# Optimization experiments

Hardware: AMD Instinct MI355X
Metric: run time of the kernel (lower is better)

The kernel has to match this reference:

```python
import jax, jax.numpy as jnp
import numpy as np

SR = 44100
D = SR * 30          # duration_samples = 1_323_000
N = 1024             # number of note events
L = 32768            # max note length in samples
W = 1024             # hann window length (module's window_length)
H = 8                # harmonics in the synth
K = 128              # FIR taps in the effect chain
LAT = 2              # time_latent_size


def setup_inputs() -> dict:
    key = jax.random.key(0)
    ks = jax.random.split(key, 10)
    freq_rad = jax.random.uniform(ks[0], (N,), jnp.float32, 0.01, 0.3)
    velocity = jax.random.uniform(ks[1], (N,), jnp.float32, 1.0, 127.0)
    starts = jax.random.randint(ks[2], (N,), 0, D - L, dtype=jnp.int32)
    lengths = jax.random.randint(ks[3], (N,), 2048, L + 1, dtype=jnp.int32)
    # time_embedder: Linear(1,32) -> ReLU -> Linear(32,LAT)
    w1 = jax.random.normal(ks[4], (1, 32), jnp.float32)
    b1 = jnp.zeros((32,), jnp.float32)
    w2 = jax.random.normal(ks[5], (32, LAT), jnp.float32) / jnp.sqrt(32.0)
    b2 = jnp.zeros((LAT,), jnp.float32)
    # synth amplitude MLP: [freq, vel, latent] (2+LAT) -> 64 -> H
    ws1 = jax.random.normal(ks[6], (2 + LAT, 64), jnp.float32)
    bs1 = jnp.zeros((64,), jnp.float32)
    ws2 = jax.random.normal(ks[7], (64, H), jnp.float32) / 8.0
    bs2 = jnp.zeros((H,), jnp.float32)
    # effect chain: causal FIR (OIW layout) + tanh
    fir = jax.random.normal(ks[8], (1, 1, K), jnp.float32) / K
    return dict(freq_rad=freq_rad, velocity=velocity,
                w1=w1, b1=b1, w2=w2, b2=b2,
                ws1=ws1, bs1=bs1, ws2=ws2, bs2=bs2, fir=fir,
                starts=starts, lengths=lengths, duration_samples=D)


def reference(freq_rad, velocity, w1, b1, w2, b2, ws1, bs1, ws2, bs2, fir,
              starts, lengths, duration_samples):
    Dn = int(duration_samples)
    t = jnp.arange(L, dtype=jnp.float32)            # [L]
    ti = jnp.arange(L, dtype=jnp.int32)             # [L]
    ends = starts + lengths
    # output_length = min(end, duration) - start, clipped to [0, L]
    out_len = jnp.clip(jnp.minimum(ends, Dn) - starts, 0, L)  # [N]
    # time latent: MLP on normalized start time
    nt = (starts.astype(jnp.float32) / Dn)[:, None]           # [N,1]
    lat = jax.nn.relu(nt @ w1 + b1) @ w2 + b2                  # [N,LAT]
    vel = (velocity / 127.0)[:, None]                          # [N,1]
    # harmonic amplitudes from tiny MLP (the 'synth')
    feat = jnp.concatenate([freq_rad[:, None], vel, lat], axis=-1)  # [N,2+LAT]
    amps = jax.nn.softplus(jax.nn.relu(feat @ ws1 + bs1) @ ws2 + bs2)  # [N,H]
    # additive synthesis; fixed small loop over harmonics, vectorized over [N,L]
    phase = freq_rad[:, None] * t[None, :]                     # [N,L]
    seg = jnp.zeros((N, L), jnp.float32)
    for hh in range(1, H + 1):
        seg = seg + amps[:, hh - 1:hh] * jnp.sin(hh * phase)
    seg = seg * vel
    # hann window (torch periodic) on the LAST W samples of each variable-length segment
    n = jnp.arange(W, dtype=jnp.float32)
    hann = 0.5 * (1.0 - jnp.cos(2.0 * jnp.pi * n / W))         # [W]
    wpos = ti[None, :] - (out_len[:, None] - W)                # [N,L]
    in_win = (wpos >= 0) & (wpos < W)
    factor = jnp.where(in_win, hann[jnp.clip(wpos, 0, W - 1)], 1.0)
    mask = (ti[None, :] < out_len[:, None]).astype(jnp.float32)  # zero past segment end
    seg = seg * factor * mask
    # effect chain: causal 128-tap FIR then tanh (masked so padding stays silent)
    y = jax.lax.conv_general_dilated(seg[:, None, :], fir,
                                     window_strides=(1,), padding=[(K - 1, 0)])
    seg = jnp.tanh(y[:, 0, :]) * mask                          # [N,L]
    # overlap-add: scatter each note into the output buffer
    idx = starts[:, None] + ti[None, :]                        # [N,L]
    valid = (ti[None, :] < out_len[:, None]) & (idx < Dn)
    contrib = jnp.where(valid, seg, 0.0)
    out = jnp.zeros((Dn,), jnp.float32).at[jnp.clip(idx, 0, Dn - 1).reshape(-1)].add(
        contrib.reshape(-1))
    return out
```

## Files before the change

kernel.cpp:

```cpp
#include <hip/hip_runtime.h>
#include <math.h>

#define LMAX  32768
#define WWIN  1024
#define KFIR  128
#define WOUT  1024
#define TO    1024
#define CPAD  1232
#define SYNTH 1152
#define ZPS   1148
#define SLOT  128

typedef _Float16 v8h __attribute__((ext_vector_type(8)));
typedef _Float16 v4h __attribute__((ext_vector_type(4)));
typedef float    v4f __attribute__((ext_vector_type(4)));
typedef float    v2f __attribute__((ext_vector_type(2)));

__device__ __forceinline__ float fast_tanh(float x) {
    float e = __builtin_amdgcn_exp2f(x * 2.8853900817779268f);
    return fmaf(-2.0f, __builtin_amdgcn_rcpf(e + 1.0f), 1.0f);
}

__global__ __launch_bounds__(256) void setup_notes_k(
    const float* __restrict__ freq_g, const float* __restrict__ velo_g,
    const float* __restrict__ w1,  const float* __restrict__ b1,
    const float* __restrict__ w2,  const float* __restrict__ b2,
    const float* __restrict__ ws1, const float* __restrict__ bs1,
    const float* __restrict__ ws2, const float* __restrict__ bs2,
    const int* __restrict__ starts, const int* __restrict__ lengths,
    float* __restrict__ npar, int* __restrict__ counts,
    unsigned short* __restrict__ lists,
    int Dn, int N, int n_tiles)
{
    __shared__ float s_w1[32], s_b1[32], s_w2[64], s_b2[2];
    __shared__ float s_ws1[256], s_bs1[64], s_ws2[512], s_bs2[8];
    const int tid = threadIdx.x;
    if (tid < 32) { s_w1[tid] = w1[tid]; s_b1[tid] = b1[tid]; }
    if (tid < 64) { s_w2[tid] = w2[tid]; s_bs1[tid] = bs1[tid]; }
    if (tid < 2)  s_b2[tid] = b2[tid];
    if (tid < 8)  s_bs2[tid] = bs2[tid];
    s_ws1[tid] = ws1[tid];
    s_ws2[tid] = ws2[tid];  s_ws2[tid + 256] = ws2[tid + 256];
    __syncthreads();

    const int j = blockIdx.x * 256 + tid;
    if (j >= N) return;

    int st  = starts[j];
    int len = lengths[j];
    int ol  = min(st + len, Dn) - st;
    ol = max(0, min(ol, LMAX));
    float v = velo_g[j] * (1.0f / 127.0f);
    float f = freq_g[j];
    float nt = (float)st / (float)Dn;
    float lat0 = s_b2[0], lat1 = s_b2[1];
    #pragma unroll
    for (int jj = 0; jj < 32; ++jj) {
        float h = fmaxf(fmaf(nt, s_w1[jj], s_b1[jj]), 0.0f);
        lat0 = fmaf(h, s_w2[jj * 2 + 0], lat0);
        lat1 = fmaf(h, s_w2[jj * 2 + 1], lat1);
    }
    float acc[8];
    #pragma unroll
    for (int h = 0; h < 8; ++h) acc[h] = s_bs2[h];
    #pragma unroll
    for (int jj = 0; jj < 64; ++jj) {
        float a = s_bs1[jj];
        a = fmaf(f,    s_ws1[0 * 64 + jj], a);
        a = fmaf(v,    s_ws1[1 * 64 + jj], a);
        a = fmaf(lat0, s_ws1[2 * 64 + jj], a);
        a = fmaf(lat1, s_ws1[3 * 64 + jj], a);
        a = fmaxf(a, 0.0f);
        #pragma unroll
        for (int h = 0; h < 8; ++h)
            acc[h] = fmaf(a, s_ws2[jj * 8 + h], acc[h]);
    }
    float* p = npar + (size_t)j * 12;
    p[0] = __int_as_float(st);
    p[1] = __int_as_float(ol);
    p[2] = f;
    p[3] = 0.0f;
    #pragma unroll
    for (int h = 0; h < 8; ++h) {
        float a = acc[h];
        float sp = fmaxf(a, 0.0f) + log1pf(expf(-fabsf(a)));
        p[4 + h] = sp * v;
    }

    if (ol > 0) {
        int t0 = st >> 10;
        int t1 = min((st + ol - 1) >> 10, n_tiles - 1);
        for (int t = t0; t <= t1; ++t) {
            int pos = atomicAdd(&counts[t], 1);
            if (pos < SLOT) lists[(size_t)t * SLOT + pos] = (unsigned short)j;
        }
    }
}

__global__ __launch_bounds__(1024) void sort_tiles_k(
    const int* __restrict__ counts, int* __restrict__ order, int n_tiles)
{
    __shared__ int hist[SLOT + 2];
    __shared__ int bstart[SLOT + 2];
    const int tid = threadIdx.x;
    if (tid < SLOT + 2) hist[tid] = 0;
    __syncthreads();
    for (int t = tid; t < n_tiles; t += 1024) {
        int k = min(counts[t], SLOT + 1);
        atomicAdd(&hist[k], 1);
    }
    __syncthreads();
    if (tid == 0) {
        int run = 0;
        for (int k = SLOT + 1; k >= 0; --k) { bstart[k] = run; run += hist[k]; }
    }
    __syncthreads();
    for (int t = tid; t < n_tiles; t += 1024) {
        int k = min(counts[t], SLOT + 1);
        int p = atomicAdd(&bstart[k], 1);
        order[p] = t;
    }
}

__global__ __launch_bounds__(256, 3) void synth_fused_k(
    const float* __restrict__ fir,
    const float* __restrict__ npar,
    const int* __restrict__ counts,
    const unsigned short* __restrict__ lists,
    const int* __restrict__ order,
    float* __restrict__ out, int Dn)
{
    __shared__ __align__(16) _Float16 segc[4][4][CPAD];
    __shared__ float fir_s[KFIR];
    __shared__ int   stl[SLOT], oll[SLOT];
    __shared__ float fl[SLOT];
    __shared__ __align__(16) float ampsl[SLOT][8];

    const int tid  = threadIdx.x;
    const int wid  = tid >> 6;
    const int lane = tid & 63;
    const int m    = lane & 15;
    const int quad = lane >> 4;
    const int grp  = wid;
    const int tile = order[blockIdx.x];
    const int o0   = tile * TO;
    const int ow   = o0;

    const int K = min(counts[tile], SLOT);

    if (tid < KFIR) fir_s[tid] = fir[tid];
    if (tid < K) {
        const int nid = (int)lists[(size_t)tile * SLOT + tid];
        const float4* pp = (const float4*)(npar + (size_t)nid * 12);
        float4 a = pp[0], b = pp[1], c = pp[2];
        stl[tid] = __float_as_int(a.x);
        oll[tid] = __float_as_int(a.y);
        fl[tid]  = a.z;
        *(float4*)&ampsl[tid][0] = b;
        *(float4*)&ampsl[tid][4] = c;
    }
    __syncthreads();

    v8h afrag[12];
    #pragma unroll
    for (int t = 0; t < 12; ++t) {
        v8h af;
        #pragma unroll
        for (int j = 0; j < 8; ++j) {
            int idx = 32 * t + 8 * quad + j - 16 * m;
            float fv = (idx >= 0 && idx < KFIR) ? fir_s[idx] : 0.0f;
            af[j] = (_Float16)fv;
        }
        afrag[t] = af;
    }
    for (int z = lane; z < 4 * (CPAD - ZPS); z += 64) {
        int S = z / (CPAD - ZPS), off = z % (CPAD - ZPS);
        segc[wid][S][ZPS + off] = (_Float16)0.0f;
    }

    const _Float16* __restrict__ bbase = &segc[wid][m & 3][(m & ~3) + 8 * quad];

    float accv[16];
    #pragma unroll
    for (int r = 0; r < 16; ++r) accv[r] = 0.0f;

    const double inv2pi = 0.15915494309189535;

    int stN = 0, olN = 0; float fN = 0.f;
    float4 amN0 = {}, amN1 = {};
    if (grp < K) {
        stN = stl[grp]; olN = oll[grp]; fN = fl[grp];
        amN0 = *(const float4*)&ampsl[grp][0];
        amN1 = *(const float4*)&ampsl[grp][4];
    }

    for (int kk = grp; kk < K; kk += 4) {
        const int st = stN, ol = olN;
        const float f = fN;
        const float4 am0 = amN0, am1 = amN1;
        if (kk + 4 < K) {
            stN = stl[kk + 4]; olN = oll[kk + 4]; fN = fl[kk + 4];
            amN0 = *(const float4*)&ampsl[kk + 4][0];
            amN1 = *(const float4*)&ampsl[kk + 4][4];
        }

        const int base = ow - st;
        if (base >= ol || base + WOUT <= 0) continue;

        const v2f A0v = {am0.x, am0.x}, A1v = {am0.y, am0.y};
        const v2f A2v = {am0.z, am0.z}, A3v = {am0.w, am0.w};
        const v2f A4v = {am1.x, am1.x}, A5v = {am1.y, am1.y};
        const v2f A6v = {am1.z, am1.z}, A7v = {am1.w, am1.w};
        const double fd = (double)f;

        const int tseed = base - 127 + lane;
        double rev0 = fd * (double)tseed * inv2pi;
        double d64  = fd * 64.0 * inv2pi;
        double rev1 = rev0 + d64;
        double d128 = d64 + d64;
        float r0   = (float)(rev0 - floor(rev0));
        float r1   = (float)(rev1 - floor(rev1));
        float r128 = (float)(d128 - floor(d128));
        v2f s  = { __builtin_amdgcn_sinf(r0), __builtin_amdgcn_sinf(r1) };
        v2f cc = { __builtin_amdgcn_cosf(r0), __builtin_amdgcn_cosf(r1) };
        const float sd128 = __builtin_amdgcn_sinf(r128);
        const float cd128 = __builtin_amdgcn_cosf(r128);
        const v2f sdv = {sd128, sd128}, cdv = {cd128, cd128};
        const int wbase = ol - WWIN;

        const bool interior = (base >= 127) && (base + WOUT + 1 <= wbase);

        if (interior) {
            #pragma unroll
            for (int j = 0; j < SYNTH / 128; ++j) {
                v2f tc = cc + cc;
                v2f sA = s;
                v2f sum = sA * A0v;
                v2f sB = tc * sA;                                 sum = __builtin_elementwise_fma(A1v, sB, sum);
                v2f sC = __builtin_elementwise_fma(tc, sB, -sA);  sum = __builtin_elementwise_fma(A2v, sC, sum);
                v2f sD = __builtin_elementwise_fma(tc, sC, -sB);  sum = __builtin_elementwise_fma(A3v, sD, sum);
                v2f sE = __builtin_elementwise_fma(tc, sD, -sC);  sum = __builtin_elementwise_fma(A4v, sE, sum);
                v2f sF = __builtin_elementwise_fma(tc, sE, -sD);  sum = __builtin_elementwise_fma(A5v, sF, sum);
                v2f sG = __builtin_elementwise_fma(tc, sF, -sE);  sum = __builtin_elementwise_fma(A6v, sG, sum);
                v2f sH = __builtin_elementwise_fma(tc, sG, -sF);  sum = __builtin_elementwise_fma(A7v, sH, sum);
                _Float16 h0 = (_Float16)sum.x;
                _Float16 h1 = (_Float16)sum.y;
                const int x0 = lane + 128 * j;
                const int x1 = x0 + 64;
                if (j == 0) {
                    #pragma unroll
                    for (int S = 0; S < 4; ++S)
                        if (x0 >= S) segc[wid][S][x0 - S] = h0;
                } else {
                    #pragma unroll
                    for (int S = 0; S < 4; ++S)
                        segc[wid][S][x0 - S] = h0;
                }
                #pragma unroll
                for (int S = 0; S < 4; ++S)
                    segc[wid][S][x1 - S] = h1;
                v2f ns = __builtin_elementwise_fma(s, cdv, cc * sdv);
                v2f nc = __builtin_elementwise_fma(cc, cdv, -(s * sdv));
                s = ns; cc = nc;
            }
        } else {
            #pragma unroll
            for (int j = 0; j < SYNTH / 128; ++j) {
                const int t0 = tseed + 128 * j;
                const int t1 = t0 + 64;
                v2f tc = cc + cc;
                v2f sA = s;
                v2f sum = sA * A0v;
                v2f sB = tc * sA;                                 sum = __builtin_elementwise_fma(A1v, sB, sum);
                v2f sC = __builtin_elementwise_fma(tc, sB, -sA);  sum = __builtin_elementwise_fma(A2v, sC, sum);
                v2f sD = __builtin_elementwise_fma(tc, sC, -sB);  sum = __builtin_elementwise_fma(A3v, sD, sum);
                v2f sE = __builtin_elementwise_fma(tc, sD, -sC);  sum = __builtin_elementwise_fma(A4v, sE, sum);
                v2f sF = __builtin_elementwise_fma(tc, sE, -sD);  sum = __builtin_elementwise_fma(A5v, sF, sum);
                v2f sG = __builtin_elementwise_fma(tc, sF, -sE);  sum = __builtin_elementwise_fma(A6v, sG, sum);
                v2f sH = __builtin_elementwise_fma(tc, sG, -sF);  sum = __builtin_elementwise_fma(A7v, sH, sum);
                float v0 = 0.0f, v1 = 0.0f;
                if (t0 >= 0 && t0 < ol) {
                    float factor = 1.0f;
                    int wpos = t0 - wbase;
                    if (wpos >= 0)
                        factor = 0.5f - 0.5f * __builtin_amdgcn_cosf((float)wpos * (1.0f / WWIN));
                    v0 = sum.x * factor;
                }
                if (t1 >= 0 && t1 < ol) {
                    float factor = 1.0f;
                    int wpos = t1 - wbase;
                    if (wpos >= 0)
                        factor = 0.5f - 0.5f * __builtin_amdgcn_cosf((float)wpos * (1.0f / WWIN));
                    v1 = sum.y * factor;
                }
                _Float16 h0 = (_Float16)v0;
                _Float16 h1 = (_Float16)v1;
                const int x0 = lane + 128 * j;
                const int x1 = x0 + 64;
                if (j == 0) {
                    #pragma unroll
                    for (int S = 0; S < 4; ++S)
                        if (x0 >= S) segc[wid][S][x0 - S] = h0;
                } else {
                    #pragma unroll
                    for (int S = 0; S < 4; ++S)
                        segc[wid][S][x0 - S] = h0;
                }
                #pragma unroll
                for (int S = 0; S < 4; ++S)
                    segc[wid][S][x1 - S] = h1;
                v2f ns = __builtin_elementwise_fma(s, cdv, cc * sdv);
                v2f nc = __builtin_elementwise_fma(cc, cdv, -(s * sdv));
                s = ns; cc = nc;
            }
        }

        #pragma unroll
        for (int p = 0; p < 2; ++p) {
            const int co = 512 * p;
            v4f CA0 = {0.f, 0.f, 0.f, 0.f};
            v4f CA1 = {0.f, 0.f, 0.f, 0.f};
            v4f CB0 = {0.f, 0.f, 0.f, 0.f};
            v4f CB1 = {0.f, 0.f, 0.f, 0.f};
            #pragma unroll
            for (int t = 0; t < 6; ++t) {
                v4h lo = *(const v4h*)(bbase + co + 32 * t);
                v4h hi = *(const v4h*)(bbase + co + 32 * t + 4);
                v8h bf = __builtin_shufflevector(lo, hi, 0, 1, 2, 3, 4, 5, 6, 7);
                CA0 = __builtin_amdgcn_mfma_f32_16x16x32_f16(afrag[t], bf, CA0, 0, 0, 0);
                v4h lo2 = *(const v4h*)(bbase + co + 256 + 32 * t);
                v4h hi2 = *(const v4h*)(bbase + co + 256 + 32 * t + 4);
                v8h bf2 = __builtin_shufflevector(lo2, hi2, 0, 1, 2, 3, 4, 5, 6, 7);
                CB0 = __builtin_amdgcn_mfma_f32_16x16x32_f16(afrag[t], bf2, CB0, 0, 0, 0);
            }
            #pragma unroll
            for (int t = 6; t < 12; ++t) {
                v4h lo = *(const v4h*)(bbase + co + 32 * t);
                v4h hi = *(const v4h*)(bbase + co + 32 * t + 4);
                v8h bf = __builtin_shufflevector(lo, hi, 0, 1, 2, 3, 4, 5, 6, 7);
                CA1 = __builtin_amdgcn_mfma_f32_16x16x32_f16(afrag[t], bf, CA1, 0, 0, 0);
                v4h lo2 = *(const v4h*)(bbase + co + 256 + 32 * t);
                v4h hi2 = *(const v4h*)(bbase + co + 256 + 32 * t + 4);
                v8h bf2 = __builtin_shufflevector(lo2, hi2, 0, 1, 2, 3, 4, 5, 6, 7);
                CB1 = __builtin_amdgcn_mfma_f32_16x16x32_f16(afrag[t], bf2, CB1, 0, 0, 0);
            }

            const int tb = base + co + 64 * quad + m;
            float y;
            y = CA0[0] + CA1[0]; if (tb +   0 >= 0 && tb +   0 < ol) accv[p*8+0] += fast_tanh(y);
            y = CA0[1] + CA1[1]; if (tb +  16 >= 0 && tb +  16 < ol) accv[p*8+1] += fast_tanh(y);
            y = CA0[2] + CA1[2]; if (tb +  32 >= 0 && tb +  32 < ol) accv[p*8+2] += fast_tanh(y);
            y = CA0[3] + CA1[3]; if (tb +  48 >= 0 && tb +  48 < ol) accv[p*8+3] += fast_tanh(y);
            y = CB0[0] + CB1[0]; if (tb + 256 >= 0 && tb + 256 < ol) accv[p*8+4] += fast_tanh(y);
            y = CB0[1] + CB1[1]; if (tb + 272 >= 0 && tb + 272 < ol) accv[p*8+5] += fast_tanh(y);
            y = CB0[2] + CB1[2]; if (tb + 288 >= 0 && tb + 288 < ol) accv[p*8+6] += fast_tanh(y);
            y = CB0[3] + CB1[3]; if (tb + 304 >= 0 && tb + 304 < ol) accv[p*8+7] += fast_tanh(y);
        }
    }

    __syncthreads();
    float* red = (float*)&segc[0][0][0];
    const int slot0 = 64 * quad + m;
    if (grp != 0) {
        float* rg = red + (grp - 1) * 1024;
        #pragma unroll
        for (int p = 0; p < 2; ++p) {
            #pragma unroll
            for (int r = 0; r < 8; ++r) {
                const int idx = slot0 + 512 * p + (r >> 2) * 256 + (r & 3) * 16;
                rg[idx] = accv[p * 8 + r];
            }
        }
    }
    __syncthreads();
    if (grp == 0) {
        #pragma unroll
        for (int p = 0; p < 2; ++p) {
            #pragma unroll
            for (int r = 0; r < 8; ++r) {
                const int idx = slot0 + 512 * p + (r >> 2) * 256 + (r & 3) * 16;
                float v = accv[p * 8 + r] + red[idx] + red[1024 + idx] + red[2048 + idx];
                const int ob = o0 + idx;
                if (ob < Dn) out[ob] = v;
            }
        }
    }
}

extern "C" void kernel_launch(void* const* d_in, const int* in_sizes, int n_in,
                              void* d_out, int out_size, void* d_ws, size_t ws_size,
                              hipStream_t stream) {
    const float* freq    = (const float*)d_in[0];
    const float* velo    = (const float*)d_in[1];
    const float* w1      = (const float*)d_in[2];
    const float* b1      = (const float*)d_in[3];
    const float* w2      = (const float*)d_in[4];
    const float* b2      = (const float*)d_in[5];
    const float* ws1     = (const float*)d_in[6];
    const float* bs1     = (const float*)d_in[7];
    const float* ws2     = (const float*)d_in[8];
    const float* bs2     = (const float*)d_in[9];
    const float* fir     = (const float*)d_in[10];
    const int*   starts  = (const int*)d_in[11];
    const int*   lengths = (const int*)d_in[12];

    const int N  = in_sizes[0];
    const int Dn = out_size;
    float* out = (float*)d_out;

    const int n_tiles = (Dn + TO - 1) / TO;

    char* ws = (char*)d_ws;
    float* npar = (float*)ws;
    size_t off1 = ((size_t)N * 12 * sizeof(float) + 255) & ~(size_t)255;
    int* counts = (int*)(ws + off1);
    size_t off2 = off1 + (((size_t)n_tiles * sizeof(int) + 255) & ~(size_t)255);
    unsigned short* lists = (unsigned short*)(ws + off2);
    size_t off3 = off2 + (((size_t)n_tiles * SLOT * sizeof(unsigned short) + 255) & ~(size_t)255);
    int* order = (int*)(ws + off3);

    hipMemsetAsync(counts, 0, (size_t)n_tiles * sizeof(int), stream);
    setup_notes_k<<<(N + 255) / 256, 256, 0, stream>>>(
        freq, velo, w1, b1, w2, b2, ws1, bs1, ws2, bs2,
        starts, lengths, npar, counts, lists, Dn, N, n_tiles);
    sort_tiles_k<<<1, 1024, 0, stream>>>(counts, order, n_tiles);
    synth_fused_k<<<n_tiles, 256, 0, stream>>>(
        fir, npar, counts, lists, order, out, Dn);
}
```

Measured before the change: 150.1 us.

## Split each note's synthesis and FIR across all four waves with double-buffered LDS

Before, each wave processed its own subset of notes over the full 1024-sample tile and the waves were combined by a shared-memory reduction at the end. Now all four waves work on every note together: each synthesizes an interleaved share of the 128-sample chunks and convolves its own 256-output quarter. A double-buffered segment buffer with one block barrier per note keeps writers and readers apart. This removes the final cross-wave reduction, roughly halves LDS use and allows a launch bound of 4 blocks, in exchange for a __syncthreads on every note and less independent work per wave between barriers.

```diff
diff --git a/kernel.cpp b/kernel.cpp
--- a/kernel.cpp
+++ b/kernel.cpp
@@ -4,7 +4,6 @@
 #define LMAX  32768
 #define WWIN  1024
 #define KFIR  128
-#define WOUT  1024
 #define TO    1024
 #define CPAD  1232
 #define SYNTH 1152
@@ -122,7 +121,7 @@
     }
 }
 
-__global__ __launch_bounds__(256, 3) void synth_fused_k(
+__global__ __launch_bounds__(256, 4) void synth_fused_k(
     const float* __restrict__ fir,
     const float* __restrict__ npar,
     const int* __restrict__ counts,
@@ -130,7 +129,7 @@
     const int* __restrict__ order,
     float* __restrict__ out, int Dn)
 {
-    __shared__ __align__(16) _Float16 segc[4][4][CPAD];
+    __shared__ __align__(16) _Float16 segc[2][4][CPAD];
     __shared__ float fir_s[KFIR];
     __shared__ int   stl[SLOT], oll[SLOT];
     __shared__ float fl[SLOT];
@@ -141,10 +140,9 @@
     const int lane = tid & 63;
     const int m    = lane & 15;
     const int quad = lane >> 4;
-    const int grp  = wid;
     const int tile = order[blockIdx.x];
     const int o0   = tile * TO;
-    const int ow   = o0;
+    const int co   = 256 * wid;
 
     const int K = min(counts[tile], SLOT);
 
@@ -173,218 +171,192 @@
         }
         afrag[t] = af;
     }
-    for (int z = lane; z < 4 * (CPAD - ZPS); z += 64) {
-        int S = z / (CPAD - ZPS), off = z % (CPAD - ZPS);
-        segc[wid][S][ZPS + off] = (_Float16)0.0f;
-    }
-
-    const _Float16* __restrict__ bbase = &segc[wid][m & 3][(m & ~3) + 8 * quad];
-
-    float accv[16];
-    #pragma unroll
-    for (int r = 0; r < 16; ++r) accv[r] = 0.0f;
-
+    for (int z = tid; z < 2 * 4 * (CPAD - ZPS); z += 256) {
+        int b = z / (4 * (CPAD - ZPS));
+        int r = z % (4 * (CPAD - ZPS));
+        int S = r / (CPAD - ZPS), off = r % (CPAD - ZPS);
+        segc[b][S][ZPS + off] = (_Float16)0.0f;
+    }
+
+    const _Float16* __restrict__ bb0 = &segc[0][m & 3][(m & ~3) + 8 * quad];
+    const _Float16* __restrict__ bb1 = &segc[1][m & 3][(m & ~3) + 8 * quad];
+
+    float accv[4] = {0.f, 0.f, 0.f, 0.f};
     const double inv2pi = 0.15915494309189535;
+    int cur = 0;
 
     int stN = 0, olN = 0; float fN = 0.f;
     float4 amN0 = {}, amN1 = {};
-    if (grp < K) {
-        stN = stl[grp]; olN = oll[grp]; fN = fl[grp];
-        amN0 = *(const float4*)&ampsl[grp][0];
-        amN1 = *(const float4*)&ampsl[grp][4];
-    }
-
-    for (int kk = grp; kk < K; kk += 4) {
+    if (K > 0) {
+        stN = stl[0]; olN = oll[0]; fN = fl[0];
+        amN0 = *(const float4*)&ampsl[0][0];
+        amN1 = *(const float4*)&ampsl[0][4];
+    }
+
+    const int nj = (wid == 0) ? 3 : 2;
+
+    for (int kk = 0; kk < K; ++kk) {
         const int st = stN, ol = olN;
         const float f = fN;
         const float4 am0 = amN0, am1 = amN1;
-        if (kk + 4 < K) {
-            stN = stl[kk + 4]; olN = oll[kk + 4]; fN = fl[kk + 4];
-            amN0 = *(const float4*)&ampsl[kk + 4][0];
-            amN1 = *(const float4*)&ampsl[kk + 4][4];
-        }
-
-        const int base = ow - st;
-        if (base >= ol || base + WOUT <= 0) continue;
+        if (kk + 1 < K) {
+            stN = stl[kk + 1]; olN = oll[kk + 1]; fN = fl[kk + 1];
+            amN0 = *(const float4*)&ampsl[kk + 1][0];
+            amN1 = *(const float4*)&ampsl[kk + 1][4];
+        }
+
+        const int base = o0 - st;
+        if (base >= ol || base + TO <= 0) continue;
 
         const v2f A0v = {am0.x, am0.x}, A1v = {am0.y, am0.y};
         const v2f A2v = {am0.z, am0.z}, A3v = {am0.w, am0.w};
         const v2f A4v = {am1.x, am1.x}, A5v = {am1.y, am1.y};
         const v2f A6v = {am1.z, am1.z}, A7v = {am1.w, am1.w};
         const double fd = (double)f;
-
-        const int tseed = base - 127 + lane;
-        double rev0 = fd * (double)tseed * inv2pi;
+        const int wbase = ol - WWIN;
+
+        const int tseed0 = base - 127 + lane + 128 * wid;
+        double rev0 = fd * (double)tseed0 * inv2pi;
         double d64  = fd * 64.0 * inv2pi;
         double rev1 = rev0 + d64;
-        double d128 = d64 + d64;
+        double d512 = fd * 512.0 * inv2pi;
         float r0   = (float)(rev0 - floor(rev0));
         float r1   = (float)(rev1 - floor(rev1));
-        float r128 = (float)(d128 - floor(d128));
+        float r512 = (float)(d512 - floor(d512));
         v2f s  = { __builtin_amdgcn_sinf(r0), __builtin_amdgcn_sinf(r1) };
         v2f cc = { __builtin_amdgcn_cosf(r0), __builtin_amdgcn_cosf(r1) };
-        const float sd128 = __builtin_amdgcn_sinf(r128);
-        const float cd128 = __builtin_amdgcn_cosf(r128);
-        const v2f sdv = {sd128, sd128}, cdv = {cd128, cd128};
-        const int wbase = ol - WWIN;
-
-        const bool interior = (base >= 127) && (base + WOUT + 1 <= wbase);
+        const float sd = __builtin_amdgcn_sinf(r512);
+        const float cd = __builtin_amdgcn_cosf(r512);
+        const v2f sdv = {sd, sd}, cdv = {cd, cd};
+
+        const bool interior = (base >= 127) && (base + TO + 1 <= wbase);
 
         if (interior) {
             #pragma unroll
-            for (int j = 0; j < SYNTH / 128; ++j) {
-                v2f tc = cc + cc;
-                v2f sA = s;
-                v2f sum = sA * A0v;
-                v2f sB = tc * sA;                                 sum = __builtin_elementwise_fma(A1v, sB, sum);
-                v2f sC = __builtin_elementwise_fma(tc, sB, -sA);  sum = __builtin_elementwise_fma(A2v, sC, sum);
-                v2f sD = __builtin_elementwise_fma(tc, sC, -sB);  sum = __builtin_elementwise_fma(A3v, sD, sum);
-                v2f sE = __builtin_elementwise_fma(tc, sD, -sC);  sum = __builtin_elementwise_fma(A4v, sE, sum);
-                v2f sF = __builtin_elementwise_fma(tc, sE, -sD);  sum = __builtin_elementwise_fma(A5v, sF, sum);
-                v2f sG = __builtin_elementwise_fma(tc, sF, -sE);  sum = __builtin_elementwise_fma(A6v, sG, sum);
-                v2f sH = __builtin_elementwise_fma(tc, sG, -sF);  sum = __builtin_elementwise_fma(A7v, sH, sum);
-                _Float16 h0 = (_Float16)sum.x;
-                _Float16 h1 = (_Float16)sum.y;
-                const int x0 = lane + 128 * j;
-                const int x1 = x0 + 64;
-                if (j == 0) {
+            for (int i = 0; i < 3; ++i) {
+                if (i < nj) {
+                    const int j = wid + 4 * i;
+                    v2f tc = cc + cc;
+                    v2f sA = s;
+                    v2f sum = sA * A0v;
+                    v2f sB = tc * sA;                                 sum = __builtin_elementwise_fma(A1v, sB, sum);
+                    v2f sC = __builtin_elementwise_fma(tc, sB, -sA);  sum = __builtin_elementwise_fma(A2v, sC, sum);
+                    v2f sD = __builtin_elementwise_fma(tc, sC, -sB);  sum = __builtin_elementwise_fma(A3v, sD, sum);
+                    v2f sE = __builtin_elementwise_fma(tc, sD, -sC);  sum = __builtin_elementwise_fma(A4v, sE, sum);
+                    v2f sF = __builtin_elementwise_fma(tc, sE, -sD);  sum = __builtin_elementwise_fma(A5v, sF, sum);
+                    v2f sG = __builtin_elementwise_fma(tc, sF, -sE);  sum = __builtin_elementwise_fma(A6v, sG, sum);
+                    v2f sH = __builtin_elementwise_fma(tc, sG, -sF);  sum = __builtin_elementwise_fma(A7v, sH, sum);
+                    _Float16 h0 = (_Float16)sum.x;
+                    _Float16 h1 = (_Float16)sum.y;
+                    const int x0 = lane + 128 * j;
+                    const int x1 = x0 + 64;
+                    if (i == 0) {
+                        #pragma unroll
+                        for (int S = 0; S < 4; ++S)
+                            if (x0 >= S) segc[cur][S][x0 - S] = h0;
+                    } else {
+                        #pragma unroll
+                        for (int S = 0; S < 4; ++S)
+                            segc[cur][S][x0 - S] = h0;
+                    }
                     #pragma unroll
                     for (int S = 0; S < 4; ++S)
-                        if (x0 >= S) segc[wid][S][x0 - S] = h0;
-                } else {
-                    #pragma unroll
-                    for (int S = 0; S < 4; ++S)
-                        segc[wid][S][x0 - S] = h0;
+                        segc[cur][S][x1 - S] = h1;
+                    v2f ns = __builtin_elementwise_fma(s, cdv, cc * sdv);
+                    v2f nc = __builtin_elementwise_fma(cc, cdv, -(s * sdv));
+                    s = ns; cc = nc;
                 }
-                #pragma unroll
-                for (int S = 0; S < 4; ++S)
-                    segc[wid][S][x1 - S] = h1;
-                v2f ns = __builtin_elementwise_fma(s, cdv, cc * sdv);
-                v2f nc = __builtin_elementwise_fma(cc, cdv, -(s * sdv));
-                s = ns; cc = nc;
             }
         } else {
             #pragma unroll
-            for (int j = 0; j < SYNTH / 128; ++j) {
-                const int t0 = tseed + 128 * j;
-                const int t1 = t0 + 64;
-                v2f tc = cc + cc;
-                v2f sA = s;
-                v2f sum = sA * A0v;
-                v2f sB = tc * sA;                                 sum = __builtin_elementwise_fma(A1v, sB, sum);
-                v2f sC = __builtin_elementwise_fma(tc, sB, -sA);  sum = __builtin_elementwise_fma(A2v, sC, sum);
-                v2f sD = __builtin_elementwise_fma(tc, sC, -sB);  sum = __builtin_elementwise_fma(A3v, sD, sum);
-                v2f sE = __builtin_elementwise_fma(tc, sD, -sC);  sum = __builtin_elementwise_fma(A4v, sE, sum);
-                v2f sF = __builtin_elementwise_fma(tc, sE, -sD);  sum = __builtin_elementwise_fma(A5v, sF, sum);
-                v2f sG = __builtin_elementwise_fma(tc, sF, -sE);  sum = __builtin_elementwise_fma(A6v, sG, sum);
-                v2f sH = __builtin_elementwise_fma(tc, sG, -sF);  sum = __builtin_elementwise_fma(A7v, sH, sum);
-                float v0 = 0.0f, v1 = 0.0f;
-                if (t0 >= 0 && t0 < ol) {
-                    float factor = 1.0f;
-                    int wpos = t0 - wbase;
-                    if (wpos >= 0)
-                        factor = 0.5f - 0.5f * __builtin_amdgcn_cosf((float)wpos * (1.0f / WWIN));
-                    v0 = sum.x * factor;
-                }
-                if (t1 >= 0 && t1 < ol) {
-                    float factor = 1.0f;
-                    int wpos = t1 - wbase;
-                    if (wpos >= 0)
-                        factor = 0.5f - 0.5f * __builtin_amdgcn_cosf((float)wpos * (1.0f / WWIN));
-                    v1 = sum.y * factor;
-                }
-                _Float16 h0 = (_Float16)v0;
-                _Float16 h1 = (_Float16)v1;
-                const int x0 = lane + 128 * j;
-                const int x1 = x0 + 64;
-                if (j == 0) {
+            for (int i = 0; i < 3; ++i) {
+                if (i < nj) {
+                    const int j = wid + 4 * i;
+                    const int t0 = tseed0 + 512 * i;
+                    const int t1 = t0 + 64;
+                    v2f tc = cc + cc;
+                    v2f sA = s;
+                    v2f sum = sA * A0v;
+                    v2f sB = tc * sA;                                 sum = __builtin_elementwise_fma(A1v, sB, sum);
+                    v2f sC = __builtin_elementwise_fma(tc, sB, -sA);  sum = __builtin_elementwise_fma(A2v, sC, sum);
+                    v2f sD = __builtin_elementwise_fma(tc, sC, -sB);  sum = __builtin_elementwise_fma(A3v, sD, sum);
+                    v2f sE = __builtin_elementwise_fma(tc, sD, -sC);  sum = __builtin_elementwise_fma(A4v, sE, sum);
+                    v2f sF = __builtin_elementwise_fma(tc, sE, -sD);  sum = __builtin_elementwise_fma(A5v, sF, sum);
+                    v2f sG = __builtin_elementwise_fma(tc, sF, -sE);  sum = __builtin_elementwise_fma(A6v, sG, sum);
+                    v2f sH = __builtin_elementwise_fma(tc, sG, -sF);  sum = __builtin_elementwise_fma(A7v, sH, sum);
+                    float v0 = 0.0f, v1 = 0.0f;
+                    if (t0 >= 0 && t0 < ol) {
+                        float factor = 1.0f;
+                        int wpos = t0 - wbase;
+                        if (wpos >= 0)
+                            factor = 0.5f - 0.5f * __builtin_amdgcn_cosf((float)wpos * (1.0f / WWIN));
+                        v0 = sum.x * factor;
+                    }
+                    if (t1 >= 0 && t1 < ol) {
+                        float factor = 1.0f;
+                        int wpos = t1 - wbase;
+                        if (wpos >= 0)
+                            factor = 0.5f - 0.5f * __builtin_amdgcn_cosf((float)wpos * (1.0f / WWIN));
+                        v1 = sum.y * factor;
+                    }
+                    _Float16 h0 = (_Float16)v0;
+                    _Float16 h1 = (_Float16)v1;
+                    const int x0 = lane + 128 * j;
+                    const int x1 = x0 + 64;
+                    if (i == 0) {
+                        #pragma unroll
+                        for (int S = 0; S < 4; ++S)
+                            if (x0 >= S) segc[cur][S][x0 - S] = h0;
+                    } else {
+                        #pragma unroll
+                        for (int S = 0; S < 4; ++S)
+                            segc[cur][S][x0 - S] = h0;
+                    }
                     #pragma unroll
                     for (int S = 0; S < 4; ++S)
-                        if (x0 >= S) segc[wid][S][x0 - S] = h0;
-                } else {
-                    #pragma unroll
-                    for (int S = 0; S < 4; ++S)
-                        segc[wid][S][x0 - S] = h0;
+                        segc[cur][S][x1 - S] = h1;
+                    v2f ns = __builtin_elementwise_fma(s, cdv, cc * sdv);
+                    v2f nc = __builtin_elementwise_fma(cc, cdv, -(s * sdv));
+                    s = ns; cc = nc;
                 }
-                #pragma unroll
-                for (int S = 0; S < 4; ++S)
-                    segc[wid][S][x1 - S] = h1;
-                v2f ns = __builtin_elementwise_fma(s, cdv, cc * sdv);
-                v2f nc = __builtin_elementwise_fma(cc, cdv, -(s * sdv));
-                s = ns; cc = nc;
             }
         }
 
+        __syncthreads();
+
+        const _Float16* __restrict__ bb = cur ? bb1 : bb0;
+        v4f CA0 = {0.f, 0.f, 0.f, 0.f};
+        v4f CA1 = {0.f, 0.f, 0.f, 0.f};
         #pragma unroll
-        for (int p = 0; p < 2; ++p) {
-            const int co = 512 * p;
-            v4f CA0 = {0.f, 0.f, 0.f, 0.f};
-            v4f CA1 = {0.f, 0.f, 0.f, 0.f};
-            v4f CB0 = {0.f, 0.f, 0.f, 0.f};
-            v4f CB1 = {0.f, 0.f, 0.f, 0.f};
-            #pragma unroll
-            for (int t = 0; t < 6; ++t) {
-                v4h lo = *(const v4h*)(bbase + co + 32 * t);
-                v4h hi = *(const v4h*)(bbase + co + 32 * t + 4);
-                v8h bf = __builtin_shufflevector(lo, hi, 0, 1, 2, 3, 4, 5, 6, 7);
-                CA0 = __builtin_amdgcn_mfma_f32_16x16x32_f16(afrag[t], bf, CA0, 0, 0, 0);
-                v4h lo2 = *(const v4h*)(bbase + co + 256 + 32 * t);
-                v4h hi2 = *(const v4h*)(bbase + co + 256 + 32 * t + 4);
-                v8h bf2 = __builtin_shufflevector(lo2, hi2, 0, 1, 2, 3, 4, 5, 6, 7);
-                CB0 = __builtin_amdgcn_mfma_f32_16x16x32_f16(afrag[t], bf2, CB0, 0, 0, 0);
-            }
-            #pragma unroll
-            for (int t = 6; t < 12; ++t) {
-                v4h lo = *(const v4h*)(bbase + co + 32 * t);
-                v4h hi = *(const v4h*)(bbase + co + 32 * t + 4);
-                v8h bf = __builtin_shufflevector(lo, hi, 0, 1, 2, 3, 4, 5, 6, 7);
-                CA1 = __builtin_amdgcn_mfma_f32_16x16x32_f16(afrag[t], bf, CA1, 0, 0, 0);
-                v4h lo2 = *(const v4h*)(bbase + co + 256 + 32 * t);
-                v4h hi2 = *(const v4h*)(bbase + co + 256 + 32 * t + 4);
-                v8h bf2 = __builtin_shufflevector(lo2, hi2, 0, 1, 2, 3, 4, 5, 6, 7);
-                CB1 = __builtin_amdgcn_mfma_f32_16x16x32_f16(afrag[t], bf2, CB1, 0, 0, 0);
-            }
-
-            const int tb = base + co + 64 * quad + m;
-            float y;
-            y = CA0[0] + CA1[0]; if (tb +   0 >= 0 && tb +   0 < ol) accv[p*8+0] += fast_tanh(y);
-            y = CA0[1] + CA1[1]; if (tb +  16 >= 0 && tb +  16 < ol) accv[p*8+1] += fast_tanh(y);
-            y = CA0[2] + CA1[2]; if (tb +  32 >= 0 && tb +  32 < ol) accv[p*8+2] += fast_tanh(y);
-            y = CA0[3] + CA1[3]; if (tb +  48 >= 0 && tb +  48 < ol) accv[p*8+3] += fast_tanh(y);
-            y = CB0[0] + CB1[0]; if (tb + 256 >= 0 && tb + 256 < ol) accv[p*8+4] += fast_tanh(y);
-            y = CB0[1] + CB1[1]; if (tb + 272 >= 0 && tb + 272 < ol) accv[p*8+5] += fast_tanh(y);
-            y = CB0[2] + CB1[2]; if (tb + 288 >= 0 && tb + 288 < ol) accv[p*8+6] += fast_tanh(y);
-            y = CB0[3] + CB1[3]; if (tb + 304 >= 0 && tb + 304 < ol) accv[p*8+7] += fast_tanh(y);
-        }
-    }
-
-    __syncthreads();
-    float* red = (float*)&segc[0][0][0];
-    const int slot0 = 64 * quad + m;
-    if (grp != 0) {
-        float* rg = red + (grp - 1) * 1024;
+        for (int t = 0; t < 6; ++t) {
+            v4h lo = *(const v4h*)(bb + co + 32 * t);
+            v4h hi = *(const v4h*)(bb + co + 32 * t + 4);
+            v8h bf = __builtin_shufflevector(lo, hi, 0, 1, 2, 3, 4, 5, 6, 7);
+            CA0 = __builtin_amdgcn_mfma_f32_16x16x32_f16(afrag[t], bf, CA0, 0, 0, 0);
+        }
         #pragma unroll
-        for (int p = 0; p < 2; ++p) {
-            #pragma unroll
-            for (int r = 0; r < 8; ++r) {
-                const int idx = slot0 + 512 * p + (r >> 2) * 256 + (r & 3) * 16;
-                rg[idx] = accv[p * 8 + r];
-            }
-        }
-    }
-    __syncthreads();
-    if (grp == 0) {
+        for (int t = 6; t < 12; ++t) {
+            v4h lo = *(const v4h*)(bb + co + 32 * t);
+            v4h hi = *(const v4h*)(bb + co + 32 * t + 4);
+            v8h bf = __builtin_shufflevector(lo, hi, 0, 1, 2, 3, 4, 5, 6, 7);
+            CA1 = __builtin_amdgcn_mfma_f32_16x16x32_f16(afrag[t], bf, CA1, 0, 0, 0);
+        }
+
+        const int tb = base + co + 64 * quad + m;
         #pragma unroll
-        for (int p = 0; p < 2; ++p) {
-            #pragma unroll
-            for (int r = 0; r < 8; ++r) {
-                const int idx = slot0 + 512 * p + (r >> 2) * 256 + (r & 3) * 16;
-                float v = accv[p * 8 + r] + red[idx] + red[1024 + idx] + red[2048 + idx];
-                const int ob = o0 + idx;
-                if (ob < Dn) out[ob] = v;
-            }
-        }
-    }
+        for (int r = 0; r < 4; ++r) {
+            float y = CA0[r] + CA1[r];
+            if ((unsigned)(tb + 16 * r) < (unsigned)ol)
+                accv[r] += fast_tanh(y);
+        }
+
+        cur ^= 1;
+    }
+
+    const int ob = o0 + co + 64 * quad + m;
+    #pragma unroll
+    for (int r = 0; r < 4; ++r)
+        if (ob + 16 * r < Dn) out[ob + 16 * r] = accv[r];
 }
 
 extern "C" void kernel_launch(void* const* d_in, const int* in_sizes, int n_in,
```

New measurement: 153.9 us. +2.6%, slower.
